# Performance work log

Measured on AMD Instinct MI355X. Metric: run time of the kernel, lower is better.

## Reference

```python
import jax, jax.numpy as jnp
import numpy as np

C = 512
NUM_HEADS = 8


def setup_inputs() -> dict:
    key = jax.random.key(0)
    ks = jax.random.split(key, 9)
    s = 1.0 / np.sqrt(C)
    inp = {
        "x": jax.random.normal(ks[0], (2, C, 64, 64), dtype=jnp.float32),
        "Wq": jax.random.uniform(ks[1], (C, C), jnp.float32, -s, s),
        "bq": jax.random.uniform(ks[2], (C,), jnp.float32, -s, s),
        "Wk": jax.random.uniform(ks[3], (C, C), jnp.float32, -s, s),
        "bk": jax.random.uniform(ks[4], (C,), jnp.float32, -s, s),
        "Wv": jax.random.uniform(ks[5], (C, C), jnp.float32, -s, s),
        "bv": jax.random.uniform(ks[6], (C,), jnp.float32, -s, s),
        "Wp": jax.random.uniform(ks[7], (C, C), jnp.float32, -s, s),
        "bp": jax.random.uniform(ks[8], (C,), jnp.float32, -s, s),
    }
    return inp


def _split_heads(t):
    # [B, S, C] -> [B, h, S, d]
    B, S, Ct = t.shape
    return t.reshape(B, S, NUM_HEADS, Ct // NUM_HEADS).transpose(0, 2, 1, 3)


def reference(x, Wq, bq, Wk, bk, Wv, bv, Wp, bp):
    B, Ct, H, W = x.shape
    tok = x.transpose(0, 2, 3, 1).reshape(B, H * W, Ct)  # [B, S, C]
    q = _split_heads(tok @ Wq.T + bq)
    k = _split_heads(tok @ Wk.T + bk)
    v = _split_heads(tok @ Wv.T + bv)
    d = q.shape[-1]
    scores = jnp.einsum("bhsd,bhtd->bhst", q, k) / jnp.sqrt(jnp.float32(d))
    attn = jax.nn.softmax(scores, axis=-1)
    out = jnp.einsum("bhst,bhtd->bhsd", attn, v)
    out = out.transpose(0, 2, 1, 3).reshape(B, H * W, Ct)  # merge heads
    out = out @ Wp.T + bp
    return out.reshape(B, H, W, Ct).transpose(0, 3, 1, 2)
```

## Files before the change

### kernel.cpp

```cpp
#include <hip/hip_runtime.h>
#include <stdint.h>
#include <math.h>

typedef unsigned short u16;
typedef uint32_t u32;
typedef short bf16x8 __attribute__((ext_vector_type(8)));
typedef float f32x4  __attribute__((ext_vector_type(4)));

#define DEV __device__ __forceinline__

DEV u16 f2bf(float f) {
    union { float f; u32 u; } x; x.f = f;
    u32 lsb = (x.u >> 16) & 1u;
    x.u += 0x7fffu + lsb;
    return (u16)(x.u >> 16);
}

DEV u32 pack2(float a, float b) {
    union { float f; u32 u; } x, y; x.f = a; y.f = b;
    return __builtin_amdgcn_perm(y.u + 0x8000u, x.u + 0x8000u, 0x07060302u);
}

#if __has_builtin(__builtin_amdgcn_exp2f)
DEV float fexp2(float x) { return __builtin_amdgcn_exp2f(x); }
#else
DEV float fexp2(float x) { return __expf(x * 0.69314718056f); }
#endif

DEV f32x4 mfma16(bf16x8 a, bf16x8 b, f32x4 c) {
    return __builtin_amdgcn_mfma_f32_16x16x32_bf16(a, b, c, 0, 0, 0);
}

__global__ __launch_bounds__(256) void prep_kernel(const float* __restrict__ x,
                                                   u16* __restrict__ tok,
                                                   const float* __restrict__ w0,
                                                   const float* __restrict__ w1,
                                                   const float* __restrict__ w2,
                                                   const float* __restrict__ w3,
                                                   u16* __restrict__ dst) {
    __shared__ u16 t[64][65];
    const int id = blockIdx.x, tid = threadIdx.x;
    if (id < 1024) {
        const int b = id >> 9, c0 = ((id >> 6) & 7) * 64, s0 = (id & 63) * 64;
        const float* xb = x + ((size_t)b * 512 + c0) * 4096 + s0;
        u16* tb = tok + ((size_t)b * 4096 + s0) * 512 + c0;
        {
            const int jc = tid & 15, i0 = tid >> 4;
#pragma unroll
            for (int ii = 0; ii < 4; ii++) {
                int i = i0 * 4 + ii;
                float4 v = *(const float4*)&xb[(size_t)i * 4096 + jc * 4];
                t[i][jc * 4 + 0] = f2bf(v.x);
                t[i][jc * 4 + 1] = f2bf(v.y);
                t[i][jc * 4 + 2] = f2bf(v.z);
                t[i][jc * 4 + 3] = f2bf(v.w);
            }
        }
        __syncthreads();
        {
            const int j = tid & 31, i0 = tid >> 5;
#pragma unroll
            for (int ii = 0; ii < 8; ii++) {
                int srow = i0 * 8 + ii;
                u32 v = (u32)t[j * 2][srow] | ((u32)t[j * 2 + 1][srow] << 16);
                *(u32*)(&tb[(size_t)srow * 512 + j * 2]) = v;
            }
        }
    } else {
        const int id2 = id - 1024;
        const int j = id2 >> 8;
        const float* src = (j == 0) ? w0 : (j == 1) ? w1 : (j == 2) ? w2 : w3;
        int idx = ((id2 & 255) * 256 + tid) * 4;
        float4 v = *(const float4*)&src[idx];
        uint2 pv;
        pv.x = pack2(v.x, v.y);
        pv.y = pack2(v.z, v.w);
        *(uint2*)&dst[(size_t)j * 262144 + idx] = pv;
    }
}

__global__ __launch_bounds__(256, 2) void qkv3_kernel(const u16* __restrict__ Wbf,
                                                      const float* __restrict__ bq,
                                                      const float* __restrict__ bk,
                                                      const float* __restrict__ bv,
                                                      const u16* __restrict__ tok,
                                                      u16* __restrict__ Qb,
                                                      u16* __restrict__ Kb,
                                                      u16* __restrict__ Vb) {
    __shared__ u16 Alds[3][6144];
    __shared__ u16 Blds[3][4096];
    const int tid = threadIdx.x;
    const int wave = tid >> 6, lane = tid & 63, q = lane >> 4, c = lane & 15;
    const int n0 = blockIdx.x * 128;
    const int m0 = blockIdx.y * 64;
    const int b  = blockIdx.z;
    const u16* tokb = tok + (size_t)b * (4096 * 512);

    const int cs = tid & 15, qs = (tid >> 4) & 3, ms = tid >> 6;
    const u16* As0 = Wbf +          (size_t)(m0 + ms * 16 + cs) * 512 + qs * 8;
    const u16* As1 = Wbf + 262144 + (size_t)(m0 + ms * 16 + cs) * 512 + qs * 8;
    const u16* As2 = Wbf + 524288 + (size_t)(m0 + ms * 16 + cs) * 512 + qs * 8;
    const u16* Bsrc0 = tokb + (size_t)(n0 + ms * 16 + cs) * 512 + qs * 8;
    const u16* Bsrc1 = tokb + (size_t)(n0 + (ms + 4) * 16 + cs) * 512 + qs * 8;

    f32x4 acc[3][2][4] = {};

    int4 pA0 = *(const int4*)&As0[0];
    int4 pA1 = *(const int4*)&As1[0];
    int4 pA2 = *(const int4*)&As2[0];
    int4 pB0 = *(const int4*)&Bsrc0[0];
    int4 pB1 = *(const int4*)&Bsrc1[0];
    int4 hA0 = *(const int4*)&As0[32];
    int4 hA1 = *(const int4*)&As1[32];
    int4 hA2 = *(const int4*)&As2[32];
    int4 hB0 = *(const int4*)&Bsrc0[32];
    int4 hB1 = *(const int4*)&Bsrc1[32];
    *(int4*)&Alds[0][tid * 8]        = pA0;
    *(int4*)&Alds[0][2048 + tid * 8] = pA1;
    *(int4*)&Alds[0][4096 + tid * 8] = pA2;
    *(int4*)&Blds[0][tid * 8]         = pB0;
    *(int4*)&Blds[0][(tid + 256) * 8] = pB1;
    __syncthreads();

    int p = 0, pw = 1;
    for (int it = 0; it < 16; it++) {
        const int kn = ((it + 2) & 15) * 32;

        int4 nA0 = *(const int4*)&As0[kn];
        int4 nA1 = *(const int4*)&As1[kn];
        int4 nA2 = *(const int4*)&As2[kn];
        int4 nB0 = *(const int4*)&Bsrc0[kn];
        int4 nB1 = *(const int4*)&Bsrc1[kn];

        bf16x8 bfr[4];
#pragma unroll
        for (int t = 0; t < 4; t++) {
            int gn = (((wave >> 1) * 4 + t) * 4 + q) * 16 + c;
            bfr[t] = *(const bf16x8*)&Blds[p][gn * 8];
        }
#pragma unroll
        for (int j = 0; j < 3; j++) {
            bf16x8 af[2];
#pragma unroll
            for (int mt = 0; mt < 2; mt++) {
                int gm = ((((wave & 1) * 2 + mt) * 4 + q) * 16 + c);
                af[mt] = *(const bf16x8*)&Alds[p][j * 2048 + gm * 8];
            }
#pragma unroll
            for (int mt = 0; mt < 2; mt++)
#pragma unroll
                for (int nt = 0; nt < 4; nt++)
                    acc[j][mt][nt] = mfma16(af[mt], bfr[nt], acc[j][mt][nt]);
        }

        *(int4*)&Alds[pw][tid * 8]        = hA0;
        *(int4*)&Alds[pw][2048 + tid * 8] = hA1;
        *(int4*)&Alds[pw][4096 + tid * 8] = hA2;
        *(int4*)&Blds[pw][tid * 8]         = hB0;
        *(int4*)&Blds[pw][(tid + 256) * 8] = hB1;
        hA0 = nA0; hA1 = nA1; hA2 = nA2; hB0 = nB0; hB1 = nB1;
        __syncthreads();
        p = pw; pw = (pw == 2) ? 0 : pw + 1;
    }

    const int mbase = m0 + (wave & 1) * 32, nbase = n0 + (wave >> 1) * 64;
    const int hd = m0 >> 6;
#pragma unroll
    for (int j = 0; j < 3; j++) {
        const float* bias = (j == 0) ? bq : (j == 1) ? bk : bv;
        const float scale = (j == 0) ? 0.1803368801f : 1.0f;
        u16* outm = (j == 0) ? Qb : Kb;
#pragma unroll
        for (int mt = 0; mt < 2; mt++) {
            int co0 = mbase + mt * 16 + q * 4;
            float b0 = bias[co0 + 0], b1 = bias[co0 + 1];
            float b2 = bias[co0 + 2], b3 = bias[co0 + 3];
#pragma unroll
            for (int nt = 0; nt < 4; nt++) {
                int scol = nbase + nt * 16 + c;
                float v0 = (acc[j][mt][nt][0] + b0) * scale;
                float v1 = (acc[j][mt][nt][1] + b1) * scale;
                float v2 = (acc[j][mt][nt][2] + b2) * scale;
                float v3 = (acc[j][mt][nt][3] + b3) * scale;
                if (j < 2) {
                    uint2 pv; pv.x = pack2(v0, v1); pv.y = pack2(v2, v3);
                    size_t idx = ((size_t)(b * 8 + hd) * 4096 + scol) * 64 + (co0 & 63);
                    *(uint2*)&outm[idx] = pv;
                } else {
                    Vb[((size_t)(b * 512 + co0 + 0)) * 4096 + scol] = f2bf(v0);
                    Vb[((size_t)(b * 512 + co0 + 1)) * 4096 + scol] = f2bf(v1);
                    Vb[((size_t)(b * 512 + co0 + 2)) * 4096 + scol] = f2bf(v2);
                    Vb[((size_t)(b * 512 + co0 + 3)) * 4096 + scol] = f2bf(v3);
                }
            }
        }
    }
}

DEV void proj_core(const u16* __restrict__ W, const float* __restrict__ bias,
                   const u16* __restrict__ Bb, void* __restrict__ out,
                   int b, int mode, float scale,
                   u16 (*__restrict__ Alds)[4096], u16 (*__restrict__ Blds)[4096]) {
    const int tid = threadIdx.x;
    const int wave = tid >> 6, lane = tid & 63, q = lane >> 4, c = lane & 15;
    const int m0 = blockIdx.y * 128, n0 = blockIdx.x * 128;

    const int cs = tid & 15, qs = (tid >> 4) & 3, ms = (tid >> 6) & 3;
    const u16* Asrc0 = W  + (size_t)(m0 + ms * 16 + cs) * 512 + qs * 8;
    const u16* Asrc1 = W  + (size_t)(m0 + (ms + 4) * 16 + cs) * 512 + qs * 8;
    const u16* Bsrc0 = Bb + (size_t)(n0 + ms * 16 + cs) * 512 + qs * 8;
    const u16* Bsrc1 = Bb + (size_t)(n0 + (ms + 4) * 16 + cs) * 512 + qs * 8;

    f32x4 acc[4][4] = {};

    int4 pa0 = *(const int4*)&Asrc0[0];
    int4 pa1 = *(const int4*)&Asrc1[0];
    int4 pb0 = *(const int4*)&Bsrc0[0];
    int4 pb1 = *(const int4*)&Bsrc1[0];
    int4 ha0 = *(const int4*)&Asrc0[32];
    int4 ha1 = *(const int4*)&Asrc1[32];
    int4 hb0 = *(const int4*)&Bsrc0[32];
    int4 hb1 = *(const int4*)&Bsrc1[32];
    *(int4*)&Alds[0][tid * 8]         = pa0;
    *(int4*)&Alds[0][(tid + 256) * 8] = pa1;
    *(int4*)&Blds[0][tid * 8]         = pb0;
    *(int4*)&Blds[0][(tid + 256) * 8] = pb1;
    __syncthreads();

    int p = 0, pw = 1;
    for (int it = 0; it < 16; it++) {
        const int kn = ((it + 2) & 15) * 32;

        int4 na0 = *(const int4*)&Asrc0[kn];
        int4 na1 = *(const int4*)&Asrc1[kn];
        int4 nb0 = *(const int4*)&Bsrc0[kn];
        int4 nb1 = *(const int4*)&Bsrc1[kn];

        bf16x8 af[4], bfr[4];
#pragma unroll
        for (int t = 0; t < 4; t++) {
            int gm = (((wave & 1) * 4 + t) * 4 + q) * 16 + c;
            af[t] = *(const bf16x8*)&Alds[p][gm * 8];
            int gn = (((wave >> 1) * 4 + t) * 4 + q) * 16 + c;
            bfr[t] = *(const bf16x8*)&Blds[p][gn * 8];
        }
#pragma unroll
        for (int mt = 0; mt < 4; mt++)
#pragma unroll
            for (int nt = 0; nt < 4; nt++)
                acc[mt][nt] = mfma16(af[mt], bfr[nt], acc[mt][nt]);

        *(int4*)&Alds[pw][tid * 8]         = ha0;
        *(int4*)&Alds[pw][(tid + 256) * 8] = ha1;
        *(int4*)&Blds[pw][tid * 8]         = hb0;
        *(int4*)&Blds[pw][(tid + 256) * 8] = hb1;
        ha0 = na0; ha1 = na1; hb0 = nb0; hb1 = nb1;
        __syncthreads();
        p = pw; pw = (pw == 2) ? 0 : pw + 1;
    }

    const int mbase = m0 + (wave & 1) * 64, nbase = n0 + (wave >> 1) * 64;
#pragma unroll
    for (int mt = 0; mt < 4; mt++) {
        int co0 = mbase + mt * 16 + q * 4;
        float b0 = bias[co0 + 0], b1 = bias[co0 + 1];
        float b2 = bias[co0 + 2], b3 = bias[co0 + 3];
#pragma unroll
        for (int nt = 0; nt < 4; nt++) {
            int scol = nbase + nt * 16 + c;
            float v0 = (acc[mt][nt][0] + b0) * scale;
            float v1 = (acc[mt][nt][1] + b1) * scale;
            float v2 = (acc[mt][nt][2] + b2) * scale;
            float v3 = (acc[mt][nt][3] + b3) * scale;
            float* o = (float*)out;
            o[((size_t)(b * 512 + co0 + 0)) * 4096 + scol] = v0;
            o[((size_t)(b * 512 + co0 + 1)) * 4096 + scol] = v1;
            o[((size_t)(b * 512 + co0 + 2)) * 4096 + scol] = v2;
            o[((size_t)(b * 512 + co0 + 3)) * 4096 + scol] = v3;
        }
    }
    (void)mode;
}

__global__ __launch_bounds__(256) void projp_kernel(const u16* __restrict__ Wp,
                                                    const float* __restrict__ bp,
                                                    const u16* __restrict__ attout,
                                                    float* __restrict__ out) {
    __shared__ u16 Alds[3][4096];
    __shared__ u16 Blds[3][4096];
    const int b = blockIdx.z;
    proj_core(Wp, bp, attout + (size_t)b * (4096 * 512), out, b, 2, 1.0f, Alds, Blds);
}

__global__ __launch_bounds__(512, 4) void attn_kernel(const u16* __restrict__ Qm,
                                                      const u16* __restrict__ Km,
                                                      const u16* __restrict__ Vm,
                                                      float* __restrict__ Opart,
                                                      float* __restrict__ Lpart) {
    __shared__ u16 Klds[2][4096];
    __shared__ u16 Vlds[2][4096];
    __shared__ u16 Plds[8][512];
    const int tid = threadIdx.x, wave = tid >> 6, lane = tid & 63;
    const int q = lane >> 4, c = lane & 15;
    const int bhd = blockIdx.y, s0 = blockIdx.x * 256, z = blockIdx.z;
    const int tbase = z * 2048;
    const u16* Qb = Qm + (size_t)bhd * (4096 * 64);
    const u16* Kb = Km + (size_t)bhd * (4096 * 64);
    const u16* Vb = Vm + (size_t)bhd * (64 * 4096);

    bf16x8 qf[2][2];
#pragma unroll
    for (int st = 0; st < 2; st++)
#pragma unroll
        for (int kd = 0; kd < 2; kd++)
            qf[st][kd] = *(const bf16x8*)
                &Qb[(size_t)(s0 + wave * 32 + st * 16 + c) * 64 + kd * 32 + q * 8];

    const int rr = tid & 15, qq = (tid >> 4) & 3, kk = (tid >> 6) & 1;
    const int t4 = tid >> 7;
    const u16* Ksrc = Kb + (size_t)(tbase + t4 * 16 + rr) * 64 + kk * 32 + qq * 8;
    const u16* Vsrc = Vb + (size_t)(t4 * 16 + rr) * 4096 + tbase + kk * 32 + qq * 8;

    u16* Pwr       = &Plds[wave][(q >> 1) * 128 + (q & 1) * 4 + c * 8];
    const u16* Prd = &Plds[wave][q * 128 + c * 8];

    f32x4 oacc[4][2] = {};
    float lsum[2] = {0.f, 0.f};

    *(int4*)&Klds[0][tid * 8] = *(const int4*)&Ksrc[0];
    *(int4*)&Vlds[0][tid * 8] = *(const int4*)&Vsrc[0];
    __syncthreads();

    for (int it = 0; it < 32; it++) {
        const int p = it & 1;
        const size_t t0n = (size_t)(((it + 1) & 31) * 64);

        int4 kst = *(const int4*)&Ksrc[t0n * 64];
        int4 vst = *(const int4*)&Vsrc[t0n];

        f32x4 sacc[4][2] = {};
#pragma unroll
        for (int kd = 0; kd < 2; kd++) {
            bf16x8 ka[4];
#pragma unroll
            for (int tt = 0; tt < 4; tt++)
                ka[tt] = *(const bf16x8*)&Klds[p][(((tt * 2 + kd) * 4 + q) * 16 + c) * 8];
#pragma unroll
            for (int tt = 0; tt < 4; tt++)
#pragma unroll
                for (int st = 0; st < 2; st++)
                    sacc[tt][st] = mfma16(ka[tt], qf[st][kd], sacc[tt][st]);
        }

        bf16x8 va[2][4];
#pragma unroll
        for (int kt = 0; kt < 2; kt++)
#pragma unroll
            for (int dt = 0; dt < 4; dt++)
                va[kt][dt] = *(const bf16x8*)&Vlds[p][(((dt * 2 + kt) * 4 + q) * 16 + c) * 8];

#pragma unroll
        for (int st = 0; st < 2; st++) {
#pragma unroll
            for (int kt = 0; kt < 2; kt++) {
#pragma unroll
                for (int t2 = 0; t2 < 2; t2++) {
                    const int tt = kt * 2 + t2;
                    float p0 = fexp2(sacc[tt][st][0]);
                    float p1 = fexp2(sacc[tt][st][1]);
                    float p2 = fexp2(sacc[tt][st][2]);
                    float p3 = fexp2(sacc[tt][st][3]);
                    lsum[st] += (p0 + p1) + (p2 + p3);
                    uint2 pv; pv.x = pack2(p0, p1); pv.y = pack2(p2, p3);
                    *(uint2*)&Pwr[t2 * 256] = pv;
                }
                bf16x8 pb = *(const bf16x8*)&Prd[0];
#pragma unroll
                for (int dt = 0; dt < 4; dt++)
                    oacc[dt][st] = mfma16(va[kt][dt], pb, oacc[dt][st]);
            }
        }

        *(int4*)&Klds[1 - p][tid * 8] = kst;
        *(int4*)&Vlds[1 - p][tid * 8] = vst;
        __syncthreads();
    }

#pragma unroll
    for (int st = 0; st < 2; st++) {
        float l = lsum[st];
        l += __shfl_xor(l, 16, 64);
        l += __shfl_xor(l, 32, 64);
        const int s = s0 + wave * 32 + st * 16 + c;
        const size_t rowbase = ((size_t)(z * 16 + bhd) * 4096 + s) * 64;
#pragma unroll
        for (int dt = 0; dt < 4; dt++) {
            float4 ov;
            ov.x = oacc[dt][st][0];
            ov.y = oacc[dt][st][1];
            ov.z = oacc[dt][st][2];
            ov.w = oacc[dt][st][3];
            *(float4*)&Opart[rowbase + dt * 16 + q * 4] = ov;
        }
        if (lane < 16)
            Lpart[(size_t)z * 65536 + bhd * 4096 + s0 + wave * 32 + st * 16 + lane] = l;
    }
}

__global__ __launch_bounds__(256) void merge_kernel(const float* __restrict__ Opart,
                                                    const float* __restrict__ Lpart,
                                                    u16* __restrict__ attout) {
    const int i = blockIdx.x * 256 + threadIdx.x;
    const int flat = i * 4;
    const int row = flat >> 6, dv = flat & 63;
    const int bhd = row >> 12, s = row & 4095;
    const float l = Lpart[row] + Lpart[65536 + row];
    const float rl = 1.0f / l;
    const float4 a  = *(const float4*)&Opart[flat];
    const float4 b4 = *(const float4*)&Opart[4194304 + flat];
    uint2 pv;
    pv.x = pack2((a.x + b4.x) * rl, (a.y + b4.y) * rl);
    pv.y = pack2((a.z + b4.z) * rl, (a.w + b4.w) * rl);
    const int b = bhd >> 3, hd = bhd & 7;
    *(uint2*)&attout[((size_t)(b * 4096 + s)) * 512 + hd * 64 + dv] = pv;
}

extern "C" void kernel_launch(void* const* d_in, const int* in_sizes, int n_in,
                              void* d_out, int out_size, void* d_ws, size_t ws_size,
                              hipStream_t stream) {
    (void)in_sizes; (void)n_in; (void)out_size; (void)ws_size;
    const float* x  = (const float*)d_in[0];
    const float* Wq = (const float*)d_in[1];
    const float* bq = (const float*)d_in[2];
    const float* Wk = (const float*)d_in[3];
    const float* bk = (const float*)d_in[4];
    const float* Wv = (const float*)d_in[5];
    const float* bv = (const float*)d_in[6];
    const float* Wp = (const float*)d_in[7];
    const float* bp = (const float*)d_in[8];
    float* out = (float*)d_out;

    const size_t NTOK = (size_t)4 * 1024 * 1024;
    u16* tok = (u16*)d_ws;
    u16* Qb  = tok + NTOK;
    u16* Kb  = Qb + NTOK;
    u16* Vb  = Kb + NTOK;
    u16* Wbf = Vb + NTOK;
    u16* attout = tok;
    float* Opart = (float*)(Wbf + 4 * 262144);
    float* Lpart = Opart + (size_t)2 * 4194304;

    prep_kernel<<<dim3(2048), 256, 0, stream>>>(x, tok, Wq, Wk, Wv, Wp, Wbf);
    qkv3_kernel<<<dim3(32, 8, 2), 256, 0, stream>>>(Wbf, bq, bk, bv, tok, Qb, Kb, Vb);
    attn_kernel<<<dim3(16, 16, 2), 512, 0, stream>>>(Qb, Kb, Vb, Opart, Lpart);
    merge_kernel<<<dim3(4096), 256, 0, stream>>>(Opart, Lpart, attout);
    projp_kernel<<<dim3(32, 4, 2), 256, 0, stream>>>(Wbf + 3 * 262144, bp, attout, out);
}
```

Measured before the change: 219.5 us.

## Fuse split-KV merge into attention kernel via last-arriving-block atomic flag

Removes the separate merge kernel. Each attention block now writes its partial output and row sums, then bumps a per-tile atomic counter. The second block to finish a tile reads the other half's partials and writes the normalized bf16 attention output directly. Flags are zeroed inside the prep kernel. This saves one kernel launch and the re-read of its own partial. In exchange it adds threadfence/atomic synchronisation and keeps the own-half partial writes, which only the other block ever reads.

```diff
diff --git a/kernel.cpp b/kernel.cpp
--- a/kernel.cpp
+++ b/kernel.cpp
@@ -37,9 +37,11 @@
                                                    const float* __restrict__ w1,
                                                    const float* __restrict__ w2,
                                                    const float* __restrict__ w3,
-                                                   u16* __restrict__ dst) {
+                                                   u16* __restrict__ dst,
+                                                   u32* __restrict__ flags) {
     __shared__ u16 t[64][65];
     const int id = blockIdx.x, tid = threadIdx.x;
+    if (id == 1024 && tid < 256) flags[tid] = 0;
     if (id < 1024) {
         const int b = id >> 9, c0 = ((id >> 6) & 7) * 64, s0 = (id & 63) * 64;
         const float* xb = x + ((size_t)b * 512 + c0) * 4096 + s0;
@@ -296,10 +298,13 @@
                                                       const u16* __restrict__ Km,
                                                       const u16* __restrict__ Vm,
                                                       float* __restrict__ Opart,
-                                                      float* __restrict__ Lpart) {
+                                                      float* __restrict__ Lpart,
+                                                      u32* __restrict__ flags,
+                                                      u16* __restrict__ attout) {
     __shared__ u16 Klds[2][4096];
     __shared__ u16 Vlds[2][4096];
     __shared__ u16 Plds[8][512];
+    __shared__ u32 whoflag;
     const int tid = threadIdx.x, wave = tid >> 6, lane = tid & 63;
     const int q = lane >> 4, c = lane & 15;
     const int bhd = blockIdx.y, s0 = blockIdx.x * 256, z = blockIdx.z;
@@ -386,11 +391,13 @@
         __syncthreads();
     }
 
+    float lown[2];
 #pragma unroll
     for (int st = 0; st < 2; st++) {
         float l = lsum[st];
         l += __shfl_xor(l, 16, 64);
         l += __shfl_xor(l, 32, 64);
+        lown[st] = l;
         const int s = s0 + wave * 32 + st * 16 + c;
         const size_t rowbase = ((size_t)(z * 16 + bhd) * 4096 + s) * 64;
 #pragma unroll
@@ -405,24 +412,36 @@
         if (lane < 16)
             Lpart[(size_t)z * 65536 + bhd * 4096 + s0 + wave * 32 + st * 16 + lane] = l;
     }
-}
-
-__global__ __launch_bounds__(256) void merge_kernel(const float* __restrict__ Opart,
-                                                    const float* __restrict__ Lpart,
-                                                    u16* __restrict__ attout) {
-    const int i = blockIdx.x * 256 + threadIdx.x;
-    const int flat = i * 4;
-    const int row = flat >> 6, dv = flat & 63;
-    const int bhd = row >> 12, s = row & 4095;
-    const float l = Lpart[row] + Lpart[65536 + row];
-    const float rl = 1.0f / l;
-    const float4 a  = *(const float4*)&Opart[flat];
-    const float4 b4 = *(const float4*)&Opart[4194304 + flat];
-    uint2 pv;
-    pv.x = pack2((a.x + b4.x) * rl, (a.y + b4.y) * rl);
-    pv.y = pack2((a.z + b4.z) * rl, (a.w + b4.w) * rl);
-    const int b = bhd >> 3, hd = bhd & 7;
-    *(uint2*)&attout[((size_t)(b * 4096 + s)) * 512 + hd * 64 + dv] = pv;
+
+    __syncthreads();
+    if (tid == 0) {
+        __threadfence();
+        whoflag = atomicAdd(&flags[bhd * 16 + blockIdx.x], 1u);
+    }
+    __syncthreads();
+
+    if (whoflag == 1) {
+        __threadfence();
+        const int zo = 1 - z;
+        const int b = bhd >> 3, hd = bhd & 7;
+#pragma unroll
+        for (int st = 0; st < 2; st++) {
+            const int s = s0 + wave * 32 + st * 16 + c;
+            const float lo = Lpart[(size_t)zo * 65536 + bhd * 4096 + s];
+            const float rl = 1.0f / (lown[st] + lo);
+            const size_t rowo = ((size_t)(zo * 16 + bhd) * 4096 + s) * 64;
+#pragma unroll
+            for (int dt = 0; dt < 4; dt++) {
+                float4 o4 = *(const float4*)&Opart[rowo + dt * 16 + q * 4];
+                uint2 pv;
+                pv.x = pack2((oacc[dt][st][0] + o4.x) * rl,
+                             (oacc[dt][st][1] + o4.y) * rl);
+                pv.y = pack2((oacc[dt][st][2] + o4.z) * rl,
+                             (oacc[dt][st][3] + o4.w) * rl);
+                *(uint2*)&attout[((size_t)(b * 4096 + s)) * 512 + hd * 64 + dt * 16 + q * 4] = pv;
+            }
+        }
+    }
 }
 
 extern "C" void kernel_launch(void* const* d_in, const int* in_sizes, int n_in,
@@ -449,10 +468,10 @@
     u16* attout = tok;
     float* Opart = (float*)(Wbf + 4 * 262144);
     float* Lpart = Opart + (size_t)2 * 4194304;
-
-    prep_kernel<<<dim3(2048), 256, 0, stream>>>(x, tok, Wq, Wk, Wv, Wp, Wbf);
+    u32* flags   = (u32*)(Lpart + (size_t)2 * 65536);
+
+    prep_kernel<<<dim3(2048), 256, 0, stream>>>(x, tok, Wq, Wk, Wv, Wp, Wbf, flags);
     qkv3_kernel<<<dim3(32, 8, 2), 256, 0, stream>>>(Wbf, bq, bk, bv, tok, Qb, Kb, Vb);
-    attn_kernel<<<dim3(16, 16, 2), 512, 0, stream>>>(Qb, Kb, Vb, Opart, Lpart);
-    merge_kernel<<<dim3(4096), 256, 0, stream>>>(Opart, Lpart, attout);
+    attn_kernel<<<dim3(16, 16, 2), 512, 0, stream>>>(Qb, Kb, Vb, Opart, Lpart, flags, attout);
     projp_kernel<<<dim3(32, 4, 2), 256, 0, stream>>>(Wbf + 3 * 262144, bp, attout, out);
 }
```

Result: slower. 303.4 us (+38.2%).
